# Optimization experiments

Measured on AMD Instinct MI355X. Metric: run time of the kernel, lower is better.

The kernel has to match this reference:

```python
import jax, jax.numpy as jnp
import numpy as np

VOCAB, EMB, UNITS, OUT = 10000, 256, 128, 2
B, T = 256, 1024


def setup_inputs() -> dict:
    key = jax.random.key(0)
    ks = jax.random.split(key, 7)
    x = jax.random.randint(ks[0], (B, T), 0, VOCAB, dtype=jnp.int32)
    emb_table = jax.random.normal(ks[1], (VOCAB, EMB), dtype=jnp.float32) * 0.05
    # Keras LSTM: kernel [EMB,4U], recurrent_kernel [U,4U], bias [4U]; gate order i,f,c,o
    Wk = jax.random.normal(ks[2], (EMB, 4 * UNITS), dtype=jnp.float32) * 0.05
    Wr = jax.random.normal(ks[3], (UNITS, 4 * UNITS), dtype=jnp.float32) * 0.05
    b = jax.random.normal(ks[4], (4 * UNITS,), dtype=jnp.float32) * 0.05
    Wd = jax.random.normal(ks[5], (UNITS, OUT), dtype=jnp.float32) * 0.05
    bd = jax.random.normal(ks[6], (OUT,), dtype=jnp.float32) * 0.05
    return {"x": x, "emb_table": emb_table, "Wk": Wk, "Wr": Wr, "b": b, "Wd": Wd, "bd": bd}


def _lstm_relu(e, Wk, Wr, b):
    # e: [B, T, EMB]. activation='relu' (cell/out), recurrent_activation=sigmoid.
    xg = jnp.einsum('bte,eg->btg', e, Wk) + b          # precompute input gates [B,T,4U]
    xg = jnp.transpose(xg, (1, 0, 2))                   # [T, B, 4U]

    def step(carry, xg_t):
        h, c = carry
        z = xg_t + h @ Wr                               # [B, 4U]
        zi, zf, zc, zo = jnp.split(z, 4, axis=-1)       # Keras gate order i,f,c,o
        i = jax.nn.sigmoid(zi)
        f = jax.nn.sigmoid(zf)
        g = jax.nn.relu(zc)
        o = jax.nn.sigmoid(zo)
        c_new = f * c + i * g
        h_new = o * jax.nn.relu(c_new)
        return (h_new, c_new), None

    batch = e.shape[0]
    h0 = jnp.zeros((batch, Wr.shape[0]), dtype=e.dtype)
    c0 = jnp.zeros((batch, Wr.shape[0]), dtype=e.dtype)
    (h_last, _), _ = jax.lax.scan(step, (h0, c0), xg)
    return h_last                                       # [B, U] (return_sequences=False)


def reference(x, emb_table, Wk, Wr, b, Wd, bd):
    e = emb_table[x]                                    # [B, T, EMB] embedding lookup
    h = _lstm_relu(e, Wk, Wr, b)                        # [B, U]
    return h @ Wd + bd                                  # [B, 2]
```

## Files before the change

### kernel.cpp

```cpp
#include <hip/hip_runtime.h>

typedef __bf16 bf16_t;
typedef __attribute__((ext_vector_type(8))) __bf16 bf16x8;
typedef __attribute__((ext_vector_type(4))) float f32x4;
typedef unsigned short u16;
typedef unsigned int u32;
typedef unsigned long long u64;

#define TC 128
#define NCH 8
#define XGHALF 16777216
#define LDA 264
#define LOG2E 1.44269504f

#define LDS_BARRIER() asm volatile("s_waitcnt lgkmcnt(0)\n\ts_barrier" ::: "memory")

#if __has_builtin(__builtin_amdgcn_exp2f)
#define EXP2F __builtin_amdgcn_exp2f
#else
static __device__ __forceinline__ float EXP2F(float x) {
  float r;
  asm volatile("v_exp_f32 %0, %1\n\ts_nop 1" : "=v"(r) : "v"(x));
  return r;
}
#endif


static __device__ __forceinline__ u16 bf16bits(float v) {
  return __builtin_bit_cast(u16, (bf16_t)v);
}
static __device__ __forceinline__ float bf16f(u16 v) {
  return __builtin_bit_cast(float, (u32)v << 16);
}

__global__ __launch_bounds__(512) void k_fused(
    const int* __restrict__ x, const float* __restrict__ emb,
    u16* __restrict__ embb, const float* __restrict__ Wk,
    u16* __restrict__ wkt, const float* __restrict__ Wr,
    u16* __restrict__ wrt, const float* __restrict__ bias,
    const float* __restrict__ Wd, const float* __restrict__ bd,
    u16* __restrict__ xg, float* __restrict__ hstf, float* __restrict__ cstf,
    float* __restrict__ out, int cs) {
  const int tid = threadIdx.x;
  const int w = tid >> 6, lane = tid & 63;
  const int l16 = lane & 15, quad = lane >> 4;

  if (cs == -2) {
    const int bid = blockIdx.x;
    if (bid >= 9) {
      for (int i = (bid - 9) * 512 + tid; i < 2560000; i += 262144)
        embb[i] = bf16bits(emb[i]);
    } else if (bid == 8) {
      const int u = 16 * w + l16;
#pragma unroll
      for (int j = 0; j < 4; ++j) {
        const float sj = (j == 2) ? 1.0f : -LOG2E;
#pragma unroll
        for (int kt = 0; kt < 4; ++kt)
#pragma unroll
          for (int jj = 0; jj < 8; ++jj)
            wrt[tid * 128 + (j * 4 + kt) * 8 + jj] =
                bf16bits(Wr[(kt * 32 + quad * 8 + jj) * 512 + u + 128 * j] * sj);
      }
    } else {
      for (int i = bid * 512 + tid; i < 131072; i += 4096) {
        int k = i & 255, n = i >> 8;
        wkt[i] = bf16bits(Wk[k * 512 + n]);
      }
    }
    return;
  }

  if (blockIdx.x >= 64) {
    const int cb = cs + 1;
    if (cb >= NCH) return;
    const int tau = blockIdx.x - 64;
    const int gg = tau >> 5, tb = tau & 31;
    u16* xgc = xg + (size_t)(cb & 1) * XGHALF;
    __shared__ u16 Al[64 * LDA];
    __shared__ float biasl[512];

    bf16x8 bfr[4][8];
#pragma unroll
    for (int nt = 0; nt < 4; ++nt) {
      const u16* bp = wkt + (64 * w + 16 * nt + l16) * 256 + quad * 8;
#pragma unroll
      for (int kt = 0; kt < 8; ++kt)
        bfr[nt][kt] = *(const bf16x8*)(bp + kt * 32);
    }

#pragma unroll
    for (int p = 0; p < 4; ++p) {
      int f = p * 512 + tid;
      int lr = f >> 5, ch = f & 31;
      int xi = (16 * gg + (lr & 15)) * 1024 + cb * TC + tb * 4 + (lr >> 4);
      int idx = x[xi];
      *(uint4*)&Al[lr * LDA + ch * 8] = *(const uint4*)&embb[idx * 256 + ch * 8];
    }
    biasl[tid] = bias[tid];
    __syncthreads();

    f32x4 acc[4][4];
#pragma unroll
    for (int mt = 0; mt < 4; ++mt)
#pragma unroll
      for (int nt = 0; nt < 4; ++nt) acc[mt][nt] = f32x4{0.f, 0.f, 0.f, 0.f};
#pragma unroll
    for (int kt = 0; kt < 8; ++kt) {
      bf16x8 a[4];
#pragma unroll
      for (int mt = 0; mt < 4; ++mt)
        a[mt] = *(const bf16x8*)&Al[(mt * 16 + l16) * LDA + kt * 32 + quad * 8];
#pragma unroll
      for (int nt = 0; nt < 4; ++nt)
#pragma unroll
        for (int mt = 0; mt < 4; ++mt)
          acc[mt][nt] = __builtin_amdgcn_mfma_f32_16x16x32_bf16(
              a[mt], bfr[nt][kt], acc[mt][nt], 0, 0, 0);
    }

    const float gsc = ((w >> 1) == 2) ? 1.0f : -LOG2E;
    const size_t gtbase = ((size_t)(4 * gg + quad) * TC + tb * 4) * 2048;
#pragma unroll
    for (int nt = 0; nt < 4; ++nt) {
      float bv = biasl[64 * w + 16 * nt + l16];
      int tile = 4 * w + nt;
#pragma unroll
      for (int mt = 0; mt < 4; ++mt) {
        u64 pk = 0;
#pragma unroll
        for (int r = 0; r < 4; ++r)
          pk |= (u64)bf16bits((acc[mt][nt][r] + bv) * gsc) << (16 * r);
        size_t off = gtbase + (size_t)mt * 2048 + tile * 64 + l16 * 4;
        *(u64*)&xgc[off] = pk;
      }
    }
  } else {
    if (cs < 0) return;
    const int g = blockIdx.x;
    const int u = 16 * w + l16;
    __shared__ __align__(16) u16 hbuf[2][4 * 144];

    __builtin_amdgcn_s_setprio(1);

    bf16x8 wf[4][4];
    {
      const u16* wp = wrt + tid * 128;
#pragma unroll
      for (int j = 0; j < 4; ++j)
#pragma unroll
        for (int kt = 0; kt < 4; ++kt)
          wf[j][kt] = *(const bf16x8*)(wp + (j * 4 + kt) * 8);
    }

    float c1 = 0.f, h1 = 0.f;
    if (cs != 0) {
      c1 = cstf[(g * 4 + quad) * 128 + u];
      h1 = hstf[(g * 4 + quad) * 128 + u];
    }
    hbuf[0][quad * 144 + u] = bf16bits(h1);

    const u16* rd0 = &hbuf[0][(l16 >> 2) * 144 + quad * 8];
    const u16* rd1 = &hbuf[1][(l16 >> 2) * 144 + quad * 8];
    u16* wr0 = &hbuf[0][quad * 144 + u];
    u16* wr1 = &hbuf[1][quad * 144 + u];

    const u16* xp = xg + (size_t)(cs & 1) * XGHALF + (size_t)g * TC * 2048 +
                    w * 64 + l16 * 4 + quad;
    u16 xq0[4], xq1[4];
#pragma unroll
    for (int j = 0; j < 4; ++j) xq0[j] = xp[j * 512];
#pragma unroll
    for (int j = 0; j < 4; ++j) xq1[j] = xp[2048 + j * 512];
    xp += 2 * 2048;

    __syncthreads();

    auto halfstep = [&](const u16* rd, u16* wr, u16* xv) {
      bf16x8 a[4];
#pragma unroll
      for (int kt = 0; kt < 4; ++kt)
        a[kt] = *(const bf16x8*)(rd + kt * 32);
      const f32x4 c0 = {0.f, 0.f, 0.f, 0.f};
      f32x4 acc[4];
#pragma unroll
      for (int j = 0; j < 4; ++j)
        acc[j] =
            __builtin_amdgcn_mfma_f32_16x16x32_bf16(a[0], wf[j][0], c0, 0, 0, 0);
#pragma unroll
      for (int kt = 1; kt < 4; ++kt)
#pragma unroll
        for (int j = 0; j < 4; ++j)
          acc[j] = __builtin_amdgcn_mfma_f32_16x16x32_bf16(a[kt], wf[j][kt],
                                                           acc[j], 0, 0, 0);
      float zi = acc[0][0] + bf16f(xv[0]);
      float zf = acc[1][0] + bf16f(xv[1]);
      float zc = acc[2][0] + bf16f(xv[2]);
      float zo = acc[3][0] + bf16f(xv[3]);
#pragma unroll
      for (int j = 0; j < 4; ++j) xv[j] = xp[j * 512];
      xp += 2048;
      float ig = __builtin_amdgcn_rcpf(1.f + EXP2F(zi));
      float fg = __builtin_amdgcn_rcpf(1.f + EXP2F(zf));
      float og = __builtin_amdgcn_rcpf(1.f + EXP2F(zo));
      float gg = fmaxf(zc, 0.f);
      c1 = fg * c1 + ig * gg;
      h1 = og * fmaxf(c1, 0.f);
      *wr = bf16bits(h1);
      LDS_BARRIER();
    };

    for (int t2 = 0; t2 < TC; t2 += 2) {
      halfstep(rd0, wr1, xq0);
      halfstep(rd1, wr0, xq1);
    }

    if (cs != NCH - 1) {
      cstf[(g * 4 + quad) * 128 + u] = c1;
      hstf[(g * 4 + quad) * 128 + u] = h1;
    } else if (tid < 8) {
      int p = tid >> 1, jo = tid & 1;
      float o = bd[jo];
      for (int k = 0; k < 128; ++k)
        o += bf16f(hbuf[0][p * 144 + k]) * Wd[k * 2 + jo];
      out[(g * 4 + p) * 2 + jo] = o;
    }
  }
}

extern "C" void kernel_launch(void* const* d_in, const int* in_sizes, int n_in,
                              void* d_out, int out_size, void* d_ws, size_t ws_size,
                              hipStream_t stream) {
  const int* x = (const int*)d_in[0];
  const float* emb = (const float*)d_in[1];
  const float* Wk = (const float*)d_in[2];
  const float* Wr = (const float*)d_in[3];
  const float* bias = (const float*)d_in[4];
  const float* Wd = (const float*)d_in[5];
  const float* bd = (const float*)d_in[6];
  float* out = (float*)d_out;
  char* ws = (char*)d_ws;
  u16* xg = (u16*)(ws);
  u16* embb = (u16*)(ws + 67108864);
  u16* wkt = (u16*)(ws + 72228864);
  float* hst = (float*)(ws + 72491008);
  float* cst = (float*)(ws + 72622080);
  u16* wrt = (u16*)(ws + 72753152);

  k_fused<<<521, 512, 0, stream>>>(x, emb, embb, Wk, wkt, Wr, wrt, bias, Wd,
                                   bd, xg, hst, cst, out, -2);
  for (int cs = -1; cs < NCH; ++cs) {
    int nwg = (cs + 1 < NCH) ? 576 : 64;
    k_fused<<<nwg, 512, 0, stream>>>(x, emb, embb, Wk, wkt, Wr, wrt, bias,
                                     Wd, bd, xg, hst, cst, out, cs);
  }
}
```

Baseline: 606.6 us.

## Interleave gate layout for 64-bit xg loads and split MFMA accumulator chains

Changes the xg layout so each recurrent thread's four gate pre-activations for one timestep are contiguous, letting the recurrent loop fetch them with a single 64-bit load instead of four scattered 16-bit loads. Deepens the xg prefetch from two to four steps to hide global latency. It also splits the 4-deep MFMA dependency chain into two independent accumulator chains that are summed at the end, shortening the serial critical path per step. In exchange, the producer side now writes scattered 16-bit stores instead of packed 64-bit stores, and more registers are held for the prefetch.

Result: slower. 711.2 us (+17.2%).

```diff
diff --git a/kernel.cpp b/kernel.cpp
--- a/kernel.cpp
+++ b/kernel.cpp
@@ -124,16 +124,14 @@
 #pragma unroll
     for (int nt = 0; nt < 4; ++nt) {
       float bv = biasl[64 * w + 16 * nt + l16];
-      int tile = 4 * w + nt;
-#pragma unroll
-      for (int mt = 0; mt < 4; ++mt) {
-        u64 pk = 0;
+      int n = 64 * w + 16 * nt + l16;
+      int j = n >> 7, uu = n & 127;
+      u16* base = xgc + gtbase + uu * 16 + j;
+#pragma unroll
+      for (int mt = 0; mt < 4; ++mt)
 #pragma unroll
         for (int r = 0; r < 4; ++r)
-          pk |= (u64)bf16bits((acc[mt][nt][r] + bv) * gsc) << (16 * r);
-        size_t off = gtbase + (size_t)mt * 2048 + tile * 64 + l16 * 4;
-        *(u64*)&xgc[off] = pk;
-      }
+          base[mt * 2048 + r * 4] = bf16bits((acc[mt][nt][r] + bv) * gsc);
     }
   } else {
     if (cs < 0) return;
@@ -165,41 +163,50 @@
     u16* wr0 = &hbuf[0][quad * 144 + u];
     u16* wr1 = &hbuf[1][quad * 144 + u];
 
-    const u16* xp = xg + (size_t)(cs & 1) * XGHALF + (size_t)g * TC * 2048 +
-                    w * 64 + l16 * 4 + quad;
-    u16 xq0[4], xq1[4];
-#pragma unroll
-    for (int j = 0; j < 4; ++j) xq0[j] = xp[j * 512];
-#pragma unroll
-    for (int j = 0; j < 4; ++j) xq1[j] = xp[2048 + j * 512];
-    xp += 2 * 2048;
+    const u16* xb = xg + (size_t)(cs & 1) * XGHALF + (size_t)g * TC * 2048 +
+                    u * 16 + quad * 4;
+    u64 xq0 = *(const u64*)(xb);
+    u64 xq1 = *(const u64*)(xb + 2048);
+    u64 xq2 = *(const u64*)(xb + 2 * 2048);
+    u64 xq3 = *(const u64*)(xb + 3 * 2048);
+    const u16* xp = xb + 4 * 2048;
 
     __syncthreads();
 
-    auto halfstep = [&](const u16* rd, u16* wr, u16* xv) {
-      bf16x8 a[4];
-#pragma unroll
-      for (int kt = 0; kt < 4; ++kt)
-        a[kt] = *(const bf16x8*)(rd + kt * 32);
+    auto halfstep = [&](const u16* rd, u16* wr, u64& xv) {
+      bf16x8 a0 = *(const bf16x8*)(rd);
+      bf16x8 a2 = *(const bf16x8*)(rd + 2 * 32);
+      bf16x8 a1 = *(const bf16x8*)(rd + 1 * 32);
+      bf16x8 a3 = *(const bf16x8*)(rd + 3 * 32);
+      u32 lo = (u32)xv, hi = (u32)(xv >> 32);
+      float x0 = __builtin_bit_cast(float, lo << 16);
+      float x1 = __builtin_bit_cast(float, lo & 0xffff0000u);
+      float x2 = __builtin_bit_cast(float, hi << 16);
+      float x3 = __builtin_bit_cast(float, hi & 0xffff0000u);
+      xv = *(const u64*)xp;
+      xp += 2048;
       const f32x4 c0 = {0.f, 0.f, 0.f, 0.f};
-      f32x4 acc[4];
-#pragma unroll
-      for (int j = 0; j < 4; ++j)
-        acc[j] =
-            __builtin_amdgcn_mfma_f32_16x16x32_bf16(a[0], wf[j][0], c0, 0, 0, 0);
-#pragma unroll
-      for (int kt = 1; kt < 4; ++kt)
-#pragma unroll
-        for (int j = 0; j < 4; ++j)
-          acc[j] = __builtin_amdgcn_mfma_f32_16x16x32_bf16(a[kt], wf[j][kt],
-                                                           acc[j], 0, 0, 0);
-      float zi = acc[0][0] + bf16f(xv[0]);
-      float zf = acc[1][0] + bf16f(xv[1]);
-      float zc = acc[2][0] + bf16f(xv[2]);
-      float zo = acc[3][0] + bf16f(xv[3]);
-#pragma unroll
-      for (int j = 0; j < 4; ++j) xv[j] = xp[j * 512];
-      xp += 2048;
+      f32x4 accA[4], accB[4];
+#pragma unroll
+      for (int j = 0; j < 4; ++j)
+        accA[j] =
+            __builtin_amdgcn_mfma_f32_16x16x32_bf16(a0, wf[j][0], c0, 0, 0, 0);
+#pragma unroll
+      for (int j = 0; j < 4; ++j)
+        accB[j] =
+            __builtin_amdgcn_mfma_f32_16x16x32_bf16(a2, wf[j][2], c0, 0, 0, 0);
+#pragma unroll
+      for (int j = 0; j < 4; ++j)
+        accA[j] = __builtin_amdgcn_mfma_f32_16x16x32_bf16(a1, wf[j][1],
+                                                          accA[j], 0, 0, 0);
+#pragma unroll
+      for (int j = 0; j < 4; ++j)
+        accB[j] = __builtin_amdgcn_mfma_f32_16x16x32_bf16(a3, wf[j][3],
+                                                          accB[j], 0, 0, 0);
+      float zi = accA[0][0] + accB[0][0] + x0;
+      float zf = accA[1][0] + accB[1][0] + x1;
+      float zc = accA[2][0] + accB[2][0] + x2;
+      float zo = accA[3][0] + accB[3][0] + x3;
       float ig = __builtin_amdgcn_rcpf(1.f + EXP2F(zi));
       float fg = __builtin_amdgcn_rcpf(1.f + EXP2F(zf));
       float og = __builtin_amdgcn_rcpf(1.f + EXP2F(zo));
@@ -210,9 +217,11 @@
       LDS_BARRIER();
     };
 
-    for (int t2 = 0; t2 < TC; t2 += 2) {
+    for (int t4 = 0; t4 < TC; t4 += 4) {
       halfstep(rd0, wr1, xq0);
       halfstep(rd1, wr0, xq1);
+      halfstep(rd0, wr1, xq2);
+      halfstep(rd1, wr0, xq3);
     }
 
     if (cs != NCH - 1) {
```
